# Kernel tuning notes

Measured on AMD Instinct MI355X. Metric: run time of the kernel, lower is better.

Reference implementation:

```python
import jax, jax.numpy as jnp
import numpy as np

B, T, I, H = 64, 2048, 64, 512
DT, TAU, NOISE_VAR = 1.0, 10.0, 0.1


def setup_inputs() -> dict:
    key = jax.random.key(0)
    k1, k2, k3, k4 = jax.random.split(key, 4)
    x = jax.random.normal(k1, (B, T, I), dtype=jnp.float32)
    # W_in: rows roughly unit-norm (original uses sparse row init normalized to L2=1)
    W_in = jax.random.normal(k2, (I, H), dtype=jnp.float32)
    W_in = W_in / jnp.linalg.norm(W_in, axis=1, keepdims=True)
    # W_hidden: randn/sqrt(H), normalized by spectral radius (as in init_W_hidden)
    Wh = np.asarray(jax.random.normal(k3, (H, H), dtype=jnp.float32)) / np.sqrt(H)
    Wh = Wh / np.max(np.abs(np.linalg.eigvals(Wh)))
    W_hidden = jnp.asarray(Wh.astype(np.float32))
    # noise drawn once per forward in the original; made an explicit input here
    sigma_all = jax.random.normal(k4, (B, T, H), dtype=jnp.float32) * NOISE_VAR
    h_0 = jnp.zeros((B, H), dtype=jnp.float32)
    return {"x": x, "W_in": W_in, "W_hidden": W_hidden, "sigma_all": sigma_all, "h_0": h_0}


def reference(x, W_in, W_hidden, sigma_all, h_0):
    c1 = jnp.float32(1.0 - DT / TAU)
    c2 = jnp.float32(DT / TAU)
    # precompute input projection for all timesteps (as the original does)
    w_input = jnp.einsum("bti,ih->bth", x, W_in)  # [B,T,H]

    def step(h, inp):
        wi_t, sg_t = inp  # each [B,H]
        h = c1 * h + c2 * (wi_t + jnp.tanh(h) @ W_hidden) + sg_t
        return h, h

    xs = (jnp.swapaxes(w_input, 0, 1), jnp.swapaxes(sigma_all, 0, 1))  # [T,B,H]
    h_f, out_t = jax.lax.scan(step, h_0, xs)
    out = jnp.swapaxes(out_t, 0, 1)  # [B,T,H]
    return out, h_f
```

## Files before the change

kernel.cpp:

```cpp
#include <hip/hip_runtime.h>
#include <hip/hip_fp16.h>

typedef _Float16 h2f   __attribute__((ext_vector_type(2)));
typedef _Float16 half8 __attribute__((ext_vector_type(8)));
typedef float    f32x4 __attribute__((ext_vector_type(4)));

#define RB 64
#define RT 2048
#define RI 64
#define RH 512
#define C1F 0.9f
#define C2F 0.1f

#define NU      64
#define PIN_KS  12
#define LDS_KS  3
#define STR_KS  1

static __device__ __forceinline__ half8 bc8(uint4 v) {
    return __builtin_bit_cast(half8, v);
}

#define MFMA(a, b, c) __builtin_amdgcn_mfma_f32_16x16x32_f16((a), (b), (c), 0, 0, 0)

__global__ void prep_pack(const float* __restrict__ W, h2f* __restrict__ P) {
    int e = blockIdx.x * 256 + threadIdx.x;
    if (e >= NU * RH * 4) return;
    int q = e & 3;
    int j = (e >> 2) & (RH - 1);
    int u = e >> 11;
    int k = 8 * u + 2 * q;
    h2f r;
    r.x = (_Float16)W[k * RH + j];
    r.y = (_Float16)W[(k + 1) * RH + j];
    P[e] = r;
}

#define WROWS 8
__global__ __launch_bounds__(512) void wis_gemm(
        const float* __restrict__ x, const float* __restrict__ Win,
        const float* __restrict__ sigma, float* __restrict__ outWIS) {
    const int j = threadIdx.x;
    const long r0 = (long)blockIdx.x * WROWS;

    float win[RI];
    #pragma unroll
    for (int i = 0; i < RI; ++i) win[i] = Win[i * RH + j];
    #pragma unroll
    for (int i = 0; i < RI; ++i) asm volatile("" : "+v"(win[i]));

    #pragma unroll
    for (int r = 0; r < WROWS; ++r) {
        const float* xr = x + (r0 + r) * RI;
        float a0 = 0.f, a1 = 0.f, a2 = 0.f, a3 = 0.f;
        #pragma unroll
        for (int i = 0; i < RI / 4; ++i) {
            a0 = fmaf(xr[4 * i + 0], win[4 * i + 0], a0);
            a1 = fmaf(xr[4 * i + 1], win[4 * i + 1], a1);
            a2 = fmaf(xr[4 * i + 2], win[4 * i + 2], a2);
            a3 = fmaf(xr[4 * i + 3], win[4 * i + 3], a3);
        }
        long idx = (r0 + r) * RH + j;
        outWIS[idx] = fmaf(C2F, (a0 + a1) + (a2 + a3), sigma[idx]);
    }
}

__global__
__attribute__((amdgpu_flat_work_group_size(512, 512), amdgpu_waves_per_eu(2, 2)))
void rnn_scan(
        const float* __restrict__ h0,
        const uint4* __restrict__ P,
        float* __restrict__ out)
{
    const int b    = blockIdx.x;
    const int tid  = threadIdx.x;
    const int wave = tid >> 6;
    const int lane = tid & 63;
    const int g    = lane >> 4;
    const int li   = lane & 15;
    const int wb   = wave * 64;
    const int col  = wb + lane;

    __shared__ __align__(16) uint4    Wl[LDS_KS * 4 * RH];
    __shared__ __align__(16) _Float16 th[2][RH];

    for (int e = tid; e < LDS_KS * 4 * RH; e += RH)
        Wl[e] = P[PIN_KS * 4 * RH + e];

    uint4 bp[PIN_KS][4];
    #pragma unroll
    for (int c = 0; c < PIN_KS; ++c)
        #pragma unroll
        for (int n = 0; n < 4; ++n)
            bp[c][n] = P[(4 * c + g) * RH + wb + n * 16 + li];
    #pragma unroll
    for (int c = 0; c < PIN_KS; ++c)
        #pragma unroll
        for (int n = 0; n < 4; ++n)
            asm volatile("" : "+v"(bp[c][n].x), "+v"(bp[c][n].y),
                               "+v"(bp[c][n].z), "+v"(bp[c][n].w));

    float* orow = out + (size_t)b * RT * RH;

    float h = h0[b * RH + col];
    {
        float e2 = __expf(2.0f * h);
        th[0][col] = (_Float16)(1.0f - 2.0f / (e2 + 1.0f));
    }
    __syncthreads();

    for (int t = 0; t < RT; ++t) {
        const uint4* thq = (const uint4*)th[t & 1];
        _Float16*    thw = th[(t & 1) ^ 1];

        float wis = orow[(size_t)t * RH + col];

        int off0 = 0;
        asm volatile("" : "+v"(off0));
        const uint4* Pst =
            P + (size_t)((PIN_KS + LDS_KS) * 4 + g) * RH + wb + li + off0;
        uint4 sf0 = Pst[0], sf1 = Pst[16], sf2 = Pst[32], sf3 = Pst[48];

        f32x4 acc0 = {0.f, 0.f, 0.f, 0.f};
        f32x4 acc1 = {0.f, 0.f, 0.f, 0.f};
        f32x4 acc2 = {0.f, 0.f, 0.f, 0.f};
        f32x4 acc3 = {0.f, 0.f, 0.f, 0.f};

        #pragma unroll
        for (int c = 0; c < PIN_KS; ++c) {
            half8 a = bc8(thq[4 * c + g]);
            acc0 = MFMA(a, bc8(bp[c][0]), acc0);
            acc1 = MFMA(a, bc8(bp[c][1]), acc1);
            acc2 = MFMA(a, bc8(bp[c][2]), acc2);
            acc3 = MFMA(a, bc8(bp[c][3]), acc3);
        }
        #pragma unroll
        for (int c = 0; c < LDS_KS; ++c) {
            half8 a = bc8(thq[4 * (PIN_KS + c) + g]);
            const uint4* wl = &Wl[(4 * c + g) * RH + wb + li];
            uint4 w0 = wl[0], w1 = wl[16], w2 = wl[32], w3 = wl[48];
            acc0 = MFMA(a, bc8(w0), acc0);
            acc1 = MFMA(a, bc8(w1), acc1);
            acc2 = MFMA(a, bc8(w2), acc2);
            acc3 = MFMA(a, bc8(w3), acc3);
        }
        {
            half8 a = bc8(thq[4 * (PIN_KS + LDS_KS) + g]);
            acc0 = MFMA(a, bc8(sf0), acc0);
            acc1 = MFMA(a, bc8(sf1), acc1);
            acc2 = MFMA(a, bc8(sf2), acc2);
            acc3 = MFMA(a, bc8(sf3), acc3);
        }

        float a = (g < 2) ? ((g == 0) ? acc0.x : acc1.x)
                          : ((g == 2) ? acc2.x : acc3.x);

        float hn = fmaf(C1F, h, fmaf(C2F, a, wis));

        float e2 = __expf(2.0f * hn);
        thw[col] = (_Float16)(1.0f - 2.0f / (e2 + 1.0f));
        orow[(size_t)t * RH + col] = hn;
        h = hn;

        asm volatile("s_waitcnt lgkmcnt(0)\n\ts_barrier" ::: "memory");
    }

    out[(size_t)RB * RT * RH + (size_t)b * RH + col] = h;
}

extern "C" void kernel_launch(void* const* d_in, const int* in_sizes, int n_in,
                              void* d_out, int out_size, void* d_ws, size_t ws_size,
                              hipStream_t stream) {
    const float* x   = (const float*)d_in[0];
    const float* Win = (const float*)d_in[1];
    const float* Wh  = (const float*)d_in[2];
    const float* sg  = (const float*)d_in[3];
    const float* h0  = (const float*)d_in[4];
    float* out = (float*)d_out;

    h2f* P = (h2f*)d_ws;

    const int n_entries = NU * RH * 4;
    hipLaunchKernelGGL(prep_pack, dim3((n_entries + 255) / 256), dim3(256), 0, stream,
                       Wh, P);
    hipLaunchKernelGGL(wis_gemm, dim3(RB * RT / WROWS), dim3(RH), 0, stream,
                       x, Win, sg, out);
    hipLaunchKernelGGL(rnn_scan, dim3(RB), dim3(RH), 0, stream,
                       h0, (const uint4*)d_ws, out);
}
```

Baseline: 3.166 ms.

## Pin all recurrent weight slices in registers and prefetch next-step input

Raises the number of register-resident W_hidden k-slices from 12 to 16. This removes the LDS-staged slices and the per-step global streamed slice, so every MFMA in the recurrence reads its B operand from registers. It also loads the next timestep's precomputed input term one iteration ahead, to hide global load latency on the serial critical path. The cost is far more register pressure: 256 VGPRs go to weights alone, under a two-waves-per-EU limit, which risks spilling.

Measured after the change: 6.337 ms. 2x slower.

```diff
diff --git a/kernel.cpp b/kernel.cpp
--- a/kernel.cpp
+++ b/kernel.cpp
@@ -13,9 +13,7 @@
 #define C2F 0.1f
 
 #define NU      64
-#define PIN_KS  12
-#define LDS_KS  3
-#define STR_KS  1
+#define PIN_KS  16
 
 static __device__ __forceinline__ half8 bc8(uint4 v) {
     return __builtin_bit_cast(half8, v);
@@ -81,11 +79,7 @@
     const int wb   = wave * 64;
     const int col  = wb + lane;
 
-    __shared__ __align__(16) uint4    Wl[LDS_KS * 4 * RH];
     __shared__ __align__(16) _Float16 th[2][RH];
-
-    for (int e = tid; e < LDS_KS * 4 * RH; e += RH)
-        Wl[e] = P[PIN_KS * 4 * RH + e];
 
     uint4 bp[PIN_KS][4];
     #pragma unroll
@@ -109,17 +103,13 @@
     }
     __syncthreads();
 
+    float wis_cur = orow[col];
+
     for (int t = 0; t < RT; ++t) {
         const uint4* thq = (const uint4*)th[t & 1];
         _Float16*    thw = th[(t & 1) ^ 1];
 
-        float wis = orow[(size_t)t * RH + col];
-
-        int off0 = 0;
-        asm volatile("" : "+v"(off0));
-        const uint4* Pst =
-            P + (size_t)((PIN_KS + LDS_KS) * 4 + g) * RH + wb + li + off0;
-        uint4 sf0 = Pst[0], sf1 = Pst[16], sf2 = Pst[32], sf3 = Pst[48];
+        float wis_nxt = orow[(size_t)((t + 1 < RT) ? t + 1 : t) * RH + col];
 
         f32x4 acc0 = {0.f, 0.f, 0.f, 0.f};
         f32x4 acc1 = {0.f, 0.f, 0.f, 0.f};
@@ -134,33 +124,17 @@
             acc2 = MFMA(a, bc8(bp[c][2]), acc2);
             acc3 = MFMA(a, bc8(bp[c][3]), acc3);
         }
-        #pragma unroll
-        for (int c = 0; c < LDS_KS; ++c) {
-            half8 a = bc8(thq[4 * (PIN_KS + c) + g]);
-            const uint4* wl = &Wl[(4 * c + g) * RH + wb + li];
-            uint4 w0 = wl[0], w1 = wl[16], w2 = wl[32], w3 = wl[48];
-            acc0 = MFMA(a, bc8(w0), acc0);
-            acc1 = MFMA(a, bc8(w1), acc1);
-            acc2 = MFMA(a, bc8(w2), acc2);
-            acc3 = MFMA(a, bc8(w3), acc3);
-        }
-        {
-            half8 a = bc8(thq[4 * (PIN_KS + LDS_KS) + g]);
-            acc0 = MFMA(a, bc8(sf0), acc0);
-            acc1 = MFMA(a, bc8(sf1), acc1);
-            acc2 = MFMA(a, bc8(sf2), acc2);
-            acc3 = MFMA(a, bc8(sf3), acc3);
-        }
 
         float a = (g < 2) ? ((g == 0) ? acc0.x : acc1.x)
                           : ((g == 2) ? acc2.x : acc3.x);
 
-        float hn = fmaf(C1F, h, fmaf(C2F, a, wis));
+        float hn = fmaf(C1F, h, fmaf(C2F, a, wis_cur));
 
         float e2 = __expf(2.0f * hn);
         thw[col] = (_Float16)(1.0f - 2.0f / (e2 + 1.0f));
         orow[(size_t)t * RH + col] = hn;
         h = hn;
+        wis_cur = wis_nxt;
 
         asm volatile("s_waitcnt lgkmcnt(0)\n\ts_barrier" ::: "memory");
     }
```
